# Performance work log

Measured on AMD Instinct MI355X. Metric: run time of the kernel, lower is better.

## Reference

```python
import jax, jax.numpy as jnp
import numpy as np

N, M, C = 262144, 1048576, 32768
ORIG, AF, NF, GH, H, NG = 200, 64, 32, 16, 128, 3


def setup_inputs() -> dict:
    key = jax.random.key(0)
    ks = jax.random.split(key, 16)
    w = lambda k, s: (jax.random.normal(k, s) * 0.02).astype(jnp.float32)
    d = {}
    d["atom_weights"] = jax.random.uniform(ks[0], (N, 1), dtype=jnp.float32)
    d["orig_atom_fea"] = jax.random.normal(ks[1], (N, ORIG), dtype=jnp.float32)
    d["nbr_fea"] = jax.random.normal(ks[2], (M, NF), dtype=jnp.float32)
    d["self_fea_idx"] = jax.random.randint(ks[3], (M,), 0, N)
    d["nbr_fea_idx"] = jax.random.randint(ks[4], (M,), 0, N)
    d["crystal_atom_idx"] = jnp.sort(jax.random.randint(ks[5], (N,), 0, C))
    d["emb_W"] = w(ks[6], (ORIG, AF)); d["emb_b"] = jnp.zeros((AF,), jnp.float32)
    d["filt_W"] = w(ks[7], (NG, 2 * AF + NF, AF)); d["filt_b"] = jnp.zeros((NG, AF), jnp.float32)
    d["core_W"] = w(ks[8], (NG, 2 * AF + NF, AF)); d["core_b"] = jnp.zeros((NG, AF), jnp.float32)
    d["bn_f_g"] = jnp.ones((NG, AF), jnp.float32); d["bn_f_b"] = jnp.zeros((NG, AF), jnp.float32)
    d["bn_c_g"] = jnp.ones((NG, AF), jnp.float32); d["bn_c_b"] = jnp.zeros((NG, AF), jnp.float32)
    d["bn_o_g"] = jnp.ones((NG, AF), jnp.float32); d["bn_o_b"] = jnp.zeros((NG, AF), jnp.float32)
    d["gate_W1"] = w(ks[9], (AF, GH)); d["gate_b1"] = jnp.zeros((GH,), jnp.float32)
    d["gate_bn_g"] = jnp.ones((GH,), jnp.float32); d["gate_bn_b"] = jnp.zeros((GH,), jnp.float32)
    d["gate_W2"] = w(ks[10], (GH, 1)); d["gate_b2"] = jnp.zeros((1,), jnp.float32)
    d["fc_W"] = w(ks[11], (AF, H)); d["fc_b"] = jnp.zeros((H,), jnp.float32)
    d["fc_bn_g"] = jnp.ones((H,), jnp.float32); d["fc_bn_b"] = jnp.zeros((H,), jnp.float32)
    d["out_W"] = w(ks[12], (H, 1)); d["out_b"] = jnp.zeros((1,), jnp.float32)
    return d


def _bn(x, g, b, eps=1e-5):
    # training-mode BatchNorm1d: batch stats over dim 0, biased variance
    return (x - x.mean(0)) / jnp.sqrt(x.var(0) + eps) * g + b


def reference(atom_weights, orig_atom_fea, nbr_fea, self_fea_idx, nbr_fea_idx, crystal_atom_idx,
              emb_W, emb_b, filt_W, filt_b, core_W, core_b,
              bn_f_g, bn_f_b, bn_c_g, bn_c_b, bn_o_g, bn_o_b,
              gate_W1, gate_b1, gate_bn_g, gate_bn_b, gate_W2, gate_b2,
              fc_W, fc_b, fc_bn_g, fc_bn_b, out_W, out_b):
    atom = orig_atom_fea @ emb_W + emb_b  # (N, AF)
    cnt = jnp.clip(jax.ops.segment_sum(jnp.ones((M,), atom.dtype), self_fea_idx, N), 1.0)
    for i in range(NG):  # message-passing layers
        total = jnp.concatenate([atom[self_fea_idx], atom[nbr_fea_idx], nbr_fea], axis=1)  # (M, 2AF+NF)
        f = jax.nn.sigmoid(_bn(total @ filt_W[i] + filt_b[i], bn_f_g[i], bn_f_b[i]))
        c = jax.nn.softplus(_bn(total @ core_W[i] + core_b[i], bn_c_g[i], bn_c_b[i]))
        mean = jax.ops.segment_sum(f * c, self_fea_idx, N) / cnt[:, None]  # scatter_mean
        atom = jax.nn.softplus(atom + _bn(mean, bn_o_g[i], bn_o_b[i]))
    # GlobalAttention pooling over crystals
    gate = jax.nn.relu(_bn(atom @ gate_W1 + gate_b1, gate_bn_g, gate_bn_b)) @ gate_W2 + gate_b2  # (N,1)
    gmax = jax.ops.segment_max(gate, crystal_atom_idx, C)
    gate = atom_weights * jnp.exp(gate - gmax[crystal_atom_idx])
    gate = gate / (jax.ops.segment_sum(gate, crystal_atom_idx, C)[crystal_atom_idx] + 1e-13)
    crys = jax.ops.segment_sum(gate * atom, crystal_atom_idx, C)  # (C, AF)
    crys = jax.nn.softplus(_bn(crys @ fc_W + fc_b, fc_bn_g, fc_bn_b))
    return crys @ out_W + out_b  # (C, 1)
```

## Files before the change

kernel.cpp:

```cpp
#include <hip/hip_runtime.h>
#include <cstdint>
#include <cstddef>

#define NATOM 262144
#define MEDGE 1048576
#define NCRY  32768

typedef __attribute__((ext_vector_type(8))) short short8v;
typedef __attribute__((ext_vector_type(4))) float f32x4;

__device__ __forceinline__ float4 ld4(const float* p){ return *reinterpret_cast<const float4*>(p); }

__device__ __forceinline__ float softplusf_(float x){
  return fmaxf(x, 0.0f) + log1pf(expf(-fabsf(x)));
}
__device__ __forceinline__ float softplus_fast(float x){
  return fmaxf(x, 0.0f) + __logf(1.0f + __expf(-fabsf(x)));
}
__device__ __forceinline__ float sigmoid_fast(float y){
  return __builtin_amdgcn_rcpf(1.0f + __expf(-y));
}

__device__ __forceinline__ unsigned short rne_bf16(float f){
  unsigned u = __float_as_uint(f);
  unsigned r = u + 0x7FFFu + ((u >> 16) & 1u);
  return (unsigned short)(r >> 16);
}
__device__ __forceinline__ float bfu(short s){
  return __uint_as_float(((unsigned)(unsigned short)s) << 16);
}

__device__ __forceinline__ unsigned fkey(float x){
  unsigned b = __float_as_uint(x);
  return (b & 0x80000000u) ? ~b : (b | 0x80000000u);
}
__device__ __forceinline__ float fkeyinv(unsigned k){
  unsigned b = (k & 0x80000000u) ? (k & 0x7fffffffu) : ~k;
  return __uint_as_float(b);
}

__device__ __forceinline__ void gll16(const void* g, void* l){
  __builtin_amdgcn_global_load_lds((const __attribute__((address_space(1))) unsigned*)g,
                                   (__attribute__((address_space(3))) unsigned*)l, 16, 0, 0);
}

#define CSB 32
__global__ __launch_bounds__(256) void colstage(const float* __restrict__ part,
                                                float* __restrict__ part2, int nb){
  int t = threadIdx.x;
  int rpb = nb / CSB;
  const float* p = part + (size_t)blockIdx.x*rpb*256 + t;
  float s = 0.f;
  #pragma unroll 4
  for (int r = 0; r < rpb; ++r) s += p[(size_t)r*256];
  part2[blockIdx.x*256 + t] = s;
}

__global__ __launch_bounds__(256) void cnt_kernel(const int* __restrict__ sidx, float* __restrict__ cnt){
  for (int m = blockIdx.x*256 + threadIdx.x; m < MEDGE; m += gridDim.x*256)
    atomicAdd(&cnt[sidx[m]], 1.0f);
}
__global__ __launch_bounds__(256) void recip_kernel(float* __restrict__ cnt){
  int n = blockIdx.x*256 + threadIdx.x;
  if (n < NATOM) cnt[n] = 1.0f / fmaxf(cnt[n], 1.0f);
}

__global__ __launch_bounds__(256) void nbrprep(const float* __restrict__ nbr, short* __restrict__ nbr_h){
  for (size_t ch = (size_t)blockIdx.x*256 + threadIdx.x; ch < (size_t)MEDGE*32/8; ch += (size_t)gridDim.x*256){
    const float* s = nbr + ch*8;
    float4 a = ld4(s), b = ld4(s+4);
    float fv[8] = {a.x,a.y,a.z,a.w,b.x,b.y,b.z,b.w};
    unsigned w[4];
    #pragma unroll
    for (int i=0;i<4;i++)
      w[i] = (unsigned)rne_bf16(fv[2*i]) | ((unsigned)rne_bf16(fv[2*i+1]) << 16);
    *(uint4*)(nbr_h + ch*8) = make_uint4(w[0],w[1],w[2],w[3]);
  }
}

__global__ __launch_bounds__(256) void wprep_embed(const float* __restrict__ embW,
                                                   short* __restrict__ Weh, short* __restrict__ Wel){
  int idx = blockIdx.x*256 + threadIdx.x;
  if (idx >= 64*224) return;
  int k = idx % 224, c = idx / 224;
  float w = (k < 200) ? embW[(size_t)k*64 + c] : 0.0f;
  unsigned u = __float_as_uint(w);
  unsigned h = u & 0xFFFF0000u;
  Weh[idx] = (short)(h >> 16);
  Wel[idx] = (short)rne_bf16(w - __uint_as_float(h));
}

__global__ __launch_bounds__(256) void embed_mfma(const float* __restrict__ orig,
                                                  const short* __restrict__ Weh,
                                                  const short* __restrict__ Wel,
                                                  const float* __restrict__ bias,
                                                  short* __restrict__ atom_h,
                                                  short* __restrict__ atom_l){
  __shared__ uint4 ab4[3208];
  char* ab = (char*)ab4;
  int t = threadIdx.x, lane = t & 63, wid = t >> 6;
  int r16 = lane & 15, g = lane >> 4;
  int col = wid*16 + r16;

  short8v Bh[7], Bl[7];
  #pragma unroll
  for (int ks = 0; ks < 7; ks++){
    int o = col*224 + ks*32 + g*8;
    Bh[ks] = *(const short8v*)(Weh + o);
    Bl[ks] = *(const short8v*)(Wel + o);
  }
  float bv = bias[col];
  int n0 = blockIdx.x * 64;
  const char* src = (const char*)orig + (size_t)n0*800;
  #pragma unroll
  for (int i = 0; i < 13; i++){
    int j = wid + i*4;
    if (j < 50) gll16(src + j*1024 + lane*16, ab + j*1024);
  }
  __syncthreads();

  #pragma unroll
  for (int grp = 0; grp < 4; grp++){
    f32x4 acc = {bv, bv, bv, bv};
    const char* arow = ab + (grp*16 + r16)*800;
    #pragma unroll
    for (int ks = 0; ks < 7; ks++){
      short8v ah, al;
      if (ks < 6 || g == 0){
        const float* f = (const float*)(arow + ks*128 + g*32);
        float4 f0 = *(const float4*)f, f1 = *(const float4*)(f+4);
        float fv[8] = {f0.x,f0.y,f0.z,f0.w,f1.x,f1.y,f1.z,f1.w};
        unsigned hw[4], lw[4];
        #pragma unroll
        for (int p = 0; p < 4; p++){
          unsigned ua = __float_as_uint(fv[2*p]), ub = __float_as_uint(fv[2*p+1]);
          unsigned ha = ua & 0xFFFF0000u, hb = ub & 0xFFFF0000u;
          hw[p] = (ha >> 16) | hb;
          lw[p] = (unsigned)rne_bf16(fv[2*p]   - __uint_as_float(ha))
                | ((unsigned)rne_bf16(fv[2*p+1] - __uint_as_float(hb)) << 16);
        }
        ah = __builtin_bit_cast(short8v, make_uint4(hw[0],hw[1],hw[2],hw[3]));
        al = __builtin_bit_cast(short8v, make_uint4(lw[0],lw[1],lw[2],lw[3]));
      } else {
        ah = (short8v)0; al = (short8v)0;
      }
      acc = __builtin_amdgcn_mfma_f32_16x16x32_bf16(ah, Bh[ks], acc, 0, 0, 0);
      acc = __builtin_amdgcn_mfma_f32_16x16x32_bf16(al, Bh[ks], acc, 0, 0, 0);
      acc = __builtin_amdgcn_mfma_f32_16x16x32_bf16(ah, Bl[ks], acc, 0, 0, 0);
    }
    int rowb = n0 + grp*16 + g*4;
    #pragma unroll
    for (int r = 0; r < 4; r++){
      float a = acc[r];
      unsigned u = __float_as_uint(a), h = u & 0xFFFF0000u;
      size_t off = (size_t)(rowb + r)*64 + col;
      atom_h[off] = (short)(h >> 16);
      atom_l[off] = (short)rne_bf16(a - __uint_as_float(h));
    }
  }
}

__global__ __launch_bounds__(256) void wprep(const float* __restrict__ filtW, const float* __restrict__ coreW,
                                             short* __restrict__ Wth, short* __restrict__ Wtl){
  int idx = blockIdx.x*256 + threadIdx.x;
  if (idx >= 3*128*160) return;
  int k = idx % 160; int rest = idx / 160; int c = rest & 127; int layer = rest >> 7;
  float w = (c < 64) ? filtW[((size_t)layer*160 + k)*64 + c] : coreW[((size_t)layer*160 + k)*64 + (c-64)];
  unsigned u = __float_as_uint(w);
  unsigned h = u & 0xFFFF0000u;
  Wth[idx] = (short)(h >> 16);
  Wtl[idx] = (short)rne_bf16(w - __uint_as_float(h));
}

#define NT_PER_BLK 8

#define MFMA_B(A,B,ACC) ACC = __builtin_amdgcn_mfma_f32_16x16x32_bf16(A, B, ACC, 0, 0, 0)

template<int PASS>
__global__ __launch_bounds__(256) void edge_mfma(
    const short* __restrict__ atom_h, const short* __restrict__ atom_l,
    const short* __restrict__ nbr_h,
    const int* __restrict__ sidx, const int* __restrict__ nidx,
    const short* __restrict__ Wth, const short* __restrict__ Wtl,
    const float* __restrict__ bfp, const float* __restrict__ bcp,
    const float* __restrict__ scale, const float* __restrict__ shift,
    float* __restrict__ partial,
    float* __restrict__ meanacc)
{
  __shared__ uint4 xb[2][36*32];
  int t = threadIdx.x, lane = t & 63, wid = t >> 6;
  int r16 = lane & 15, g = lane >> 4;
  int colf = wid*16 + r16, colc = colf + 64;
  int el = lane & 31;

  short8v Bhf[5], Blf[5], Bhc[5], Blc[5];
  {
    const short* wfh = Wth + colf*160;
    const short* wch = Wth + colc*160;
    const short* wfl = Wtl + colf*160;
    const short* wcl = Wtl + colc*160;
    #pragma unroll
    for (int ks = 0; ks < 5; ks++){
      int o = ks*32 + g*8;
      Bhf[ks] = *(const short8v*)(wfh + o);
      Bhc[ks] = *(const short8v*)(wch + o);
      Blf[ks] = *(const short8v*)(wfl + o);
      Blc[ks] = *(const short8v*)(wcl + o);
    }
  }
  float bfv = bfp[colf], bcv = bcp[colf];
  float sf = 0.f, hf = 0.f, sc = 0.f, hc = 0.f;
  if (PASS == 1){ sf = scale[colf]; hf = shift[colf]; sc = scale[colc]; hc = shift[colc]; }
  float s0 = 0.f, q0 = 0.f, s1 = 0.f, q1 = 0.f;

  int tile0 = blockIdx.x * NT_PER_BLK;

  #define STAGE(BUF, TILE, SE, NE)                                              \
  {                                                                             \
    uint4* dst = (uint4*)(BUF);                                                 \
    int e0s_ = (TILE)*32;                                                       \
    _Pragma("unroll")                                                           \
    for (int j = wid; j < 18; j += 4){                                          \
      int c = 2*j + (lane >> 5);                                                \
      const short* src;                                                         \
      if      (c < 8)  src = atom_h + (size_t)(SE)*64 + c*8;                    \
      else if (c < 16) src = atom_h + (size_t)(NE)*64 + (c-8)*8;                \
      else if (c < 20) src = nbr_h + (size_t)(e0s_+el)*32 + (c-16)*8;           \
      else if (c < 28) src = atom_l + (size_t)(SE)*64 + (c-20)*8;               \
      else             src = atom_l + (size_t)(NE)*64 + (c-28)*8;               \
      gll16(src, dst + j*64);                                                   \
    }                                                                           \
  }

  int se, ne;
  { int e = tile0*32 + el; se = sidx[e]; ne = nidx[e]; }
  STAGE(xb[0], tile0, se, ne);
  { int e = (tile0+1)*32 + el; se = sidx[e]; ne = nidx[e]; }

  for (int tt = 0; tt < NT_PER_BLK; ++tt){
    asm volatile("s_waitcnt vmcnt(0)" ::: "memory");
    __builtin_amdgcn_s_barrier();
    if (tt+1 < NT_PER_BLK){
      STAGE(xb[(tt+1)&1], tile0+tt+1, se, ne);
      if (tt+2 < NT_PER_BLK){ int e = (tile0+tt+2)*32 + el; se = sidx[e]; ne = nidx[e]; }
    }
    int e0 = (tile0+tt)*32;
    const char* buf = (const char*)xb[tt & 1];
    #pragma unroll
    for (int grp = 0; grp < 2; ++grp){
      f32x4 accf = {bfv,bfv,bfv,bfv}, accc = {bcv,bcv,bcv,bcv};
      const char* base = buf + (grp*16 + r16)*16;
      #pragma unroll
      for (int ks = 0; ks < 5; ++ks){
        short8v ah = *(const short8v*)(base + (ks*4+g)*512);
        MFMA_B(ah, Bhf[ks], accf); MFMA_B(ah, Bhc[ks], accc);
        MFMA_B(ah, Blf[ks], accf); MFMA_B(ah, Blc[ks], accc);
        if (ks < 4){
          short8v al = *(const short8v*)(base + (20+ks*4+g)*512);
          MFMA_B(al, Bhf[ks], accf); MFMA_B(al, Bhc[ks], accc);
        }
      }
      if (PASS == 0){
        #pragma unroll
        for (int r = 0; r < 4; r++){
          float yf = accf[r], yc = accc[r];
          s0 += yf; q0 += yf*yf; s1 += yc; q1 += yc*yc;
        }
      } else {
        int ebase = e0 + grp*16 + g*4;
        #pragma unroll
        for (int r = 0; r < 4; r++){
          float f  = sigmoid_fast(accf[r]*sf + hf);
          float c2 = softplus_fast(accc[r]*sc + hc);
          atomicAdd(&meanacc[(size_t)sidx[ebase + r]*64 + colf], f*c2);
        }
      }
    }
  }
  #undef STAGE

  if (PASS == 0){
    s0 += __shfl_xor(s0,16); s0 += __shfl_xor(s0,32);
    q0 += __shfl_xor(q0,16); q0 += __shfl_xor(q0,32);
    s1 += __shfl_xor(s1,16); s1 += __shfl_xor(s1,32);
    q1 += __shfl_xor(q1,16); q1 += __shfl_xor(q1,32);
    __syncthreads();
    float* scm = (float*)&xb[0][0];
    if (g == 0)
      *(float4*)&scm[(wid*16 + r16)*4] = make_float4(s0, q0, s1, q1);
    __syncthreads();
    {
      int stat = t >> 7, colx = t & 127;
      int isc = (colx >= 64) ? 1 : 0;
      int cc = colx & 63;
      int v = isc*2 + stat;
      partial[(size_t)blockIdx.x*256 + stat*128 + (colx & 127) - stat*0] =
          scm[((cc>>4)*16 + (cc&15))*4 + v];
    }
  }
}

__global__ void bnfin_kernel(int nf, float invcnt, const float* __restrict__ p2,
                             const float* __restrict__ g, const float* __restrict__ b,
                             float* __restrict__ scale, float* __restrict__ shift){
  int j = threadIdx.x;
  if (j >= nf) return;
  float s = 0.f, q = 0.f;
  #pragma unroll 4
  for (int r = 0; r < CSB; ++r){
    s += p2[r*256 + j];
    q += p2[r*256 + 128 + j];
  }
  float m = s*invcnt;
  float v = fmaxf(q*invcnt - m*m, 0.0f);
  float is = rsqrtf(v + 1e-5f);
  float sc = g[j]*is;
  scale[j] = sc;
  shift[j] = b[j] - m*sc;
}

__global__ void bnfin2_kernel(float invcnt, const float* __restrict__ p2,
                              const float* __restrict__ g0, const float* __restrict__ b0,
                              const float* __restrict__ g1, const float* __restrict__ b1,
                              float* __restrict__ scale, float* __restrict__ shift){
  int j = threadIdx.x;
  float s = 0.f, q = 0.f;
  #pragma unroll 4
  for (int r = 0; r < CSB; ++r){
    s += p2[r*256 + j];
    q += p2[r*256 + 128 + j];
  }
  float m = s*invcnt;
  float v = fmaxf(q*invcnt - m*m, 0.0f);
  float is = rsqrtf(v + 1e-5f);
  float gg = (j < 64) ? g0[j] : g1[j-64];
  float bb = (j < 64) ? b0[j] : b1[j-64];
  float sc = gg*is;
  scale[j] = sc;
  shift[j] = bb - m*sc;
}

__global__ __launch_bounds__(256) void meanbn_stats(const float* __restrict__ recip,
                                                    const float* __restrict__ meanacc,
                                                    float* __restrict__ partial){
  int t = threadIdx.x;
  float s = 0.f, q = 0.f;
  for (size_t idx = (size_t)blockIdx.x*256 + t; idx < (size_t)NATOM*64; idx += (size_t)gridDim.x*256){
    int n = (int)(idx >> 6);
    float v = meanacc[idx]*recip[n];
    s += v; q += v*v;
  }
  __shared__ float red[256][2];
  red[t][0]=s; red[t][1]=q;
  __syncthreads();
  if (t < 64){
    for (int i=1;i<4;i++){ s += red[t+64*i][0]; q += red[t+64*i][1]; }
    partial[(size_t)blockIdx.x*256 + t]       = s;
    partial[(size_t)blockIdx.x*256 + 128 + t] = q;
  }
}

__global__ __launch_bounds__(256) void atom_update(short* __restrict__ atom_h,
                                                   short* __restrict__ atom_l,
                                                   const float* __restrict__ meanacc,
                                                   const float* __restrict__ recip,
                                                   const float* __restrict__ scale,
                                                   const float* __restrict__ shift){
  for (size_t idx = (size_t)blockIdx.x*256 + threadIdx.x; idx < (size_t)NATOM*64; idx += (size_t)gridDim.x*256){
    int n = (int)(idx >> 6), j = (int)(idx & 63);
    float prev = bfu(atom_h[idx]) + bfu(atom_l[idx]);
    float a = softplus_fast(prev + meanacc[idx]*recip[n]*scale[j] + shift[j]);
    unsigned u = __float_as_uint(a), h = u & 0xFFFF0000u;
    atom_h[idx] = (short)(h >> 16);
    atom_l[idx] = (short)rne_bf16(a - __uint_as_float(h));
  }
}

__global__ __launch_bounds__(256, 2) void gate_pass1(const short* __restrict__ atom_h,
                                                     const short* __restrict__ atom_l,
                                                     const float* __restrict__ W1, const float* __restrict__ b1,
                                                     float* __restrict__ hbuf,
                                                     float* __restrict__ partial){
  __shared__ float As[256*65];
  __shared__ float Wl[64*16];
  int t = threadIdx.x;
  *(float4*)&Wl[t*4] = ld4(W1 + t*4);
  const short* hsrc = atom_h + (size_t)blockIdx.x*256*64;
  const short* lsrc = atom_l + (size_t)blockIdx.x*256*64;
  #pragma unroll
  for (int j = 0; j < 8; j++){
    int idx = j*256 + t;
    uint4 hv = *(const uint4*)(hsrc + idx*8);
    uint4 lv = *(const uint4*)(lsrc + idx*8);
    int r = idx >> 3, c = (idx & 7)*8;
    float* d = &As[r*65 + c];
    unsigned hw[4] = {hv.x,hv.y,hv.z,hv.w}, lw[4] = {lv.x,lv.y,lv.z,lv.w};
    #pragma unroll
    for (int i = 0; i < 4; i++){
      d[2*i]   = __uint_as_float(hw[i] << 16)          + __uint_as_float(lw[i] << 16);
      d[2*i+1] = __uint_as_float(hw[i] & 0xFFFF0000u)  + __uint_as_float(lw[i] & 0xFFFF0000u);
    }
  }
  __syncthreads();
  float h[16];
  #pragma unroll
  for (int c=0;c<16;c++) h[c] = b1[c];
  const float* ar = &As[t*65];
  #pragma unroll 8
  for (int k=0;k<64;k++){
    float a = ar[k];
    #pragma unroll
    for (int c=0;c<16;c++) h[c] += a*Wl[k*16+c];
  }
  size_t n = (size_t)blockIdx.x*256 + t;
  #pragma unroll
  for (int c=0;c<16;c+=4)
    *(float4*)&hbuf[n*16+c] = make_float4(h[c],h[c+1],h[c+2],h[c+3]);
  __syncthreads();
  #pragma unroll
  for (int c=0;c<16;c++){
    float v = h[c], v2 = h[c]*h[c];
    for (int off=32; off; off>>=1){ v += __shfl_down(v,off); v2 += __shfl_down(v2,off); }
    if ((t&63)==0){ As[(t>>6)*32 + c] = v; As[(t>>6)*32 + 16 + c] = v2; }
  }
  __syncthreads();
  if (t < 32){
    float v = As[t] + As[32+t] + As[64+t] + As[96+t];
    int col = (t < 16) ? t : (128 + t - 16);
    partial[(size_t)blockIdx.x*256 + col] = v;
  }
}

__global__ __launch_bounds__(256) void gate_pass2(const float* __restrict__ hbuf,
                                                  const float* __restrict__ scale, const float* __restrict__ shift,
                                                  const float* __restrict__ W2, const float* __restrict__ b2,
                                                  const int* __restrict__ cry,
                                                  float* __restrict__ gate, unsigned* __restrict__ gmaxk){
  int n = blockIdx.x*256 + threadIdx.x;
  float g = b2[0];
  #pragma unroll
  for (int c=0;c<16;c+=4){
    float4 hv = ld4(hbuf + (size_t)n*16 + c);
    float4 sc = ld4(scale + c), sh = ld4(shift + c), w = ld4(W2 + c);
    g += fmaxf(hv.x*sc.x+sh.x,0.f)*w.x + fmaxf(hv.y*sc.y+sh.y,0.f)*w.y
       + fmaxf(hv.z*sc.z+sh.z,0.f)*w.z + fmaxf(hv.w*sc.w+sh.w,0.f)*w.w;
  }
  gate[n] = g;
  atomicMax(&gmaxk[cry[n]], fkey(g));
}

__global__ __launch_bounds__(256) void gate_exp(float* __restrict__ gate,
                                                const float* __restrict__ aw,
                                                const int* __restrict__ cry,
                                                const unsigned* __restrict__ gmaxk,
                                                float* __restrict__ gsum){
  int n = blockIdx.x*256 + threadIdx.x;
  if (n < NATOM){
    int c = cry[n];
    float w = aw[n]*expf(gate[n] - fkeyinv(gmaxk[c]));
    gate[n] = w;
    atomicAdd(&gsum[c], w);
  }
}

__global__ __launch_bounds__(256) void crys_acc(const float* __restrict__ gate,
                                                const float* __restrict__ gsum,
                                                const int* __restrict__ cry,
                                                const short* __restrict__ atom_h,
                                                const short* __restrict__ atom_l,
                                                float* __restrict__ crys){
  for (size_t idx = (size_t)blockIdx.x*256 + threadIdx.x; idx < (size_t)NATOM*64; idx += (size_t)gridDim.x*256){
    int n = (int)(idx >> 6), j = (int)(idx & 63);
    int c = cry[n];
    float wn = gate[n] / (gsum[c] + 1e-13f);
    float a = bfu(atom_h[idx]) + bfu(atom_l[idx]);
    atomicAdd(&crys[(size_t)c*64 + j], wn*a);
  }
}

__global__ __launch_bounds__(512) void fc_stats(const float* __restrict__ crys,
                                                const float* __restrict__ fcW, const float* __restrict__ fcb,
                                                float* __restrict__ hid,
                                                float* __restrict__ partial){
  __shared__ float Wl[64*128];
  __shared__ float cb[64][16];
  int t = threadIdx.x;
  for (int j = t; j < 64*32; j += 512)
    *(float4*)&Wl[j*4] = ld4(fcW + j*4);
  int cg = t & 31, cr = t >> 5;
  float4 bias = ld4(fcb + cg*4);
  float ssum[4] = {0,0,0,0}, ssq[4] = {0,0,0,0};
  for (int chunk = blockIdx.x; chunk < NCRY/16; chunk += gridDim.x){
    int c0 = chunk*16;
    __syncthreads();
    for (int j = t; j < 256; j += 512){
      int rr = j & 15, c = j >> 4;
      float4 v = ld4(crys + (size_t)(c0+rr)*64 + c*4);
      int k = c*4;
      cb[k][rr]=v.x; cb[k+1][rr]=v.y; cb[k+2][rr]=v.z; cb[k+3][rr]=v.w;
    }
    __syncthreads();
    float4 acc = bias;
    #pragma unroll 4
    for (int k=0;k<64;k++){
      float a = cb[k][cr];
      float4 w = *(float4*)&Wl[k*128 + cg*4];
      acc.x += a*w.x; acc.y += a*w.y; acc.z += a*w.z; acc.w += a*w.w;
    }
    *(float4*)&hid[(size_t)(c0+cr)*128 + cg*4] = acc;
    ssum[0]+=acc.x; ssum[1]+=acc.y; ssum[2]+=acc.z; ssum[3]+=acc.w;
    ssq[0]+=acc.x*acc.x; ssq[1]+=acc.y*acc.y; ssq[2]+=acc.z*acc.z; ssq[3]+=acc.w*acc.w;
  }
  __syncthreads();
  float* red = Wl;
  #pragma unroll
  for (int q=0;q<4;q++){ red[t*8+q] = ssum[q]; red[t*8+4+q] = ssq[q]; }
  __syncthreads();
  if (t < 128){
    int cgj = t >> 2, q = t & 3;
    float s = 0.f, sq = 0.f;
    for (int cri=0; cri<16; cri++){
      int tt = cri*32 + cgj;
      s  += red[tt*8+q];
      sq += red[tt*8+4+q];
    }
    partial[(size_t)blockIdx.x*256 + t]       = s;
    partial[(size_t)blockIdx.x*256 + 128 + t] = sq;
  }
}

__global__ __launch_bounds__(256) void out_kernel(const float* __restrict__ hid,
                                                  const float* __restrict__ scale, const float* __restrict__ shift,
                                                  const float* __restrict__ outW, const float* __restrict__ outb,
                                                  float* __restrict__ out){
  int c = blockIdx.x*4 + (threadIdx.x >> 6);
  int l = threadIdx.x & 63;
  float v = softplusf_(hid[(size_t)c*128 + l]*scale[l] + shift[l])*outW[l]
          + softplusf_(hid[(size_t)c*128 + 64 + l]*scale[64+l] + shift[64+l])*outW[64+l];
  for (int off=32; off; off >>= 1) v += __shfl_down(v, off);
  if (l == 0) out[c] = v + outb[0];
}

extern "C" void kernel_launch(void* const* d_in, const int* in_sizes, int n_in,
                              void* d_out, int out_size, void* d_ws, size_t ws_size,
                              hipStream_t stream){
  const float* aw    = (const float*)d_in[0];
  const float* orig  = (const float*)d_in[1];
  const float* nbr   = (const float*)d_in[2];
  const int*   sidx  = (const int*)d_in[3];
  const int*   nidx  = (const int*)d_in[4];
  const int*   cry   = (const int*)d_in[5];
  const float* embW  = (const float*)d_in[6];
  const float* embB  = (const float*)d_in[7];
  const float* filtW = (const float*)d_in[8];
  const float* filtB = (const float*)d_in[9];
  const float* coreW = (const float*)d_in[10];
  const float* coreB = (const float*)d_in[11];
  const float* bnfg  = (const float*)d_in[12];
  const float* bnfb  = (const float*)d_in[13];
  const float* bncg  = (const float*)d_in[14];
  const float* bncb  = (const float*)d_in[15];
  const float* bnog  = (const float*)d_in[16];
  const float* bnob  = (const float*)d_in[17];
  const float* gW1   = (const float*)d_in[18];
  const float* gb1   = (const float*)d_in[19];
  const float* gbng  = (const float*)d_in[20];
  const float* gbnb  = (const float*)d_in[21];
  const float* gW2   = (const float*)d_in[22];
  const float* gb2   = (const float*)d_in[23];
  const float* fcW   = (const float*)d_in[24];
  const float* fcb   = (const float*)d_in[25];
  const float* fcbng = (const float*)d_in[26];
  const float* fcbnb = (const float*)d_in[27];
  const float* outW  = (const float*)d_in[28];
  const float* outb  = (const float*)d_in[29];
  float* out = (float*)d_out;

  float* ws      = (float*)d_ws;
  float* meanacc = ws;
  float* cnt     = meanacc + (size_t)NATOM*64;
  float* gate    = cnt     + NATOM;
  float* gmaxk   = gate    + NATOM;
  float* gsum    = gmaxk   + NCRY;
  float* crys    = gsum    + NCRY;
  float* hid     = crys    + (size_t)NCRY*64;
  float* part2   = hid     + (size_t)NCRY*128;
  float* scale   = part2   + 32*256;
  float* shift   = scale   + 128;
  short* wth     = (short*)(shift + 128);
  short* wtl     = wth + 3*128*160;
  float* partial = (float*)(wtl + 3*128*160);
  short* atom_h  = (short*)(partial + 4096*256);
  short* atom_l  = atom_h + (size_t)NATOM*64;
  short* nbr_h   = atom_l + (size_t)NATOM*64;
  short* weh     = nbr_h + (size_t)MEDGE*32;
  short* wel     = weh + 64*224;
  (void)in_sizes; (void)n_in; (void)out_size; (void)ws_size;

  hipMemsetAsync(cnt, 0, NATOM*sizeof(float), stream);
  cnt_kernel<<<2048, 256, 0, stream>>>(sidx, cnt);
  recip_kernel<<<NATOM/256, 256, 0, stream>>>(cnt);
  wprep<<<240, 256, 0, stream>>>(filtW, coreW, wth, wtl);
  wprep_embed<<<56, 256, 0, stream>>>(embW, weh, wel);
  nbrprep<<<2048, 256, 0, stream>>>(nbr, nbr_h);
  embed_mfma<<<NATOM/64, 256, 0, stream>>>(orig, weh, wel, embB, atom_h, atom_l);

  for (int i = 0; i < 3; ++i){
    const short* wthL = wth + (size_t)i*128*160;
    const short* wtlL = wtl + (size_t)i*128*160;
    const float* bf = filtB + i*64;
    const float* bc = coreB + i*64;
    edge_mfma<0><<<4096, 256, 0, stream>>>(atom_h, atom_l, nbr_h, sidx, nidx, wthL, wtlL, bf, bc,
                                           nullptr, nullptr, partial, nullptr);
    colstage<<<CSB, 256, 0, stream>>>(partial, part2, 4096);
    bnfin2_kernel<<<1, 128, 0, stream>>>(1.0f/MEDGE, part2,
                                         bnfg+i*64, bnfb+i*64, bncg+i*64, bncb+i*64, scale, shift);
    hipMemsetAsync(meanacc, 0, (size_t)NATOM*64*sizeof(float), stream);
    edge_mfma<1><<<4096, 256, 0, stream>>>(atom_h, atom_l, nbr_h, sidx, nidx, wthL, wtlL, bf, bc,
                                           scale, shift, nullptr, meanacc);
    meanbn_stats<<<2048, 256, 0, stream>>>(cnt, meanacc, partial);
    colstage<<<CSB, 256, 0, stream>>>(partial, part2, 2048);
    bnfin_kernel<<<1, 64, 0, stream>>>(64, 1.0f/NATOM, part2, bnog+i*64, bnob+i*64, scale, shift);
    atom_update<<<2048, 256, 0, stream>>>(atom_h, atom_l, meanacc, cnt, scale, shift);
  }

  float* hbuf = meanacc;
  gate_pass1<<<NATOM/256, 256, 0, stream>>>(atom_h, atom_l, gW1, gb1, hbuf, partial);
  colstage<<<CSB, 256, 0, stream>>>(partial, part2, NATOM/256);
  bnfin_kernel<<<1, 16, 0, stream>>>(16, 1.0f/NATOM, part2, gbng, gbnb, scale, shift);
  hipMemsetAsync(gmaxk, 0, NCRY*sizeof(unsigned), stream);
  gate_pass2<<<NATOM/256, 256, 0, stream>>>(hbuf, scale, shift, gW2, gb2, cry, gate, (unsigned*)gmaxk);
  hipMemsetAsync(gsum, 0, NCRY*sizeof(float), stream);
  gate_exp<<<NATOM/256, 256, 0, stream>>>(gate, aw, cry, (const unsigned*)gmaxk, gsum);
  hipMemsetAsync(crys, 0, (size_t)NCRY*64*sizeof(float), stream);
  crys_acc<<<4096, 256, 0, stream>>>(gate, gsum, cry, atom_h, atom_l, crys);

  fc_stats<<<1024, 512, 0, stream>>>(crys, fcW, fcb, hid, partial);
  colstage<<<CSB, 256, 0, stream>>>(partial, part2, 1024);
  bnfin_kernel<<<1, 128, 0, stream>>>(128, 1.0f/NCRY, part2, fcbng, fcbnb, scale, shift);
  out_kernel<<<NCRY/4, 256, 0, stream>>>(hid, scale, shift, outW, outb, out);
}
```

Before: 1.597 ms.

## Counting-sort edges by destination atom before message-passing layers

Adds a histogram, a three-stage prefix scan and a ranking scatter that reorder edge indices and bf16 neighbor features by self index. The edge kernels then read the sorted arrays, so gathers of self-atom rows become sequential and the scatter-mean atomics land on nearby addresses. This costs an extra pass over all edge features plus several small launches, and the order within each atom's group is nondeterministic, which can change floating-point summation order.

Measured after the change: 2.279 ms. 42.7% more time.

```diff
diff --git a/kernel.cpp b/kernel.cpp
--- a/kernel.cpp
+++ b/kernel.cpp
@@ -56,13 +56,73 @@
   part2[blockIdx.x*256 + t] = s;
 }
 
-__global__ __launch_bounds__(256) void cnt_kernel(const int* __restrict__ sidx, float* __restrict__ cnt){
+__global__ __launch_bounds__(256) void hist_kernel(const int* __restrict__ sidx, int* __restrict__ cnti){
   for (int m = blockIdx.x*256 + threadIdx.x; m < MEDGE; m += gridDim.x*256)
-    atomicAdd(&cnt[sidx[m]], 1.0f);
-}
-__global__ __launch_bounds__(256) void recip_kernel(float* __restrict__ cnt){
+    atomicAdd(&cnti[sidx[m]], 1);
+}
+
+__global__ __launch_bounds__(256) void scan1(const int* __restrict__ cnti,
+                                             int* __restrict__ loc, int* __restrict__ bsum){
+  __shared__ int sm[256];
+  int t = threadIdx.x;
+  int v = cnti[blockIdx.x*256 + t];
+  sm[t] = v;
+  __syncthreads();
+  for (int off = 1; off < 256; off <<= 1){
+    int x = (t >= off) ? sm[t-off] : 0;
+    __syncthreads();
+    sm[t] += x;
+    __syncthreads();
+  }
+  loc[blockIdx.x*256 + t] = sm[t] - v;
+  if (t == 255) bsum[blockIdx.x] = sm[255];
+}
+
+__global__ __launch_bounds__(256) void scan2(int* __restrict__ bsum){
+  __shared__ int sm[256];
+  int t = threadIdx.x;
+  int v0 = bsum[t*4+0], v1 = bsum[t*4+1], v2 = bsum[t*4+2], v3 = bsum[t*4+3];
+  int tot = v0+v1+v2+v3;
+  sm[t] = tot;
+  __syncthreads();
+  for (int off = 1; off < 256; off <<= 1){
+    int x = (t >= off) ? sm[t-off] : 0;
+    __syncthreads();
+    sm[t] += x;
+    __syncthreads();
+  }
+  int te = sm[t] - tot;
+  bsum[t*4+0] = te;
+  bsum[t*4+1] = te + v0;
+  bsum[t*4+2] = te + v0 + v1;
+  bsum[t*4+3] = te + v0 + v1 + v2;
+}
+
+__global__ __launch_bounds__(256) void scan3(const int* __restrict__ loc, const int* __restrict__ bsum,
+                                             int* __restrict__ base){
+  int i = blockIdx.x*256 + threadIdx.x;
+  base[i] = loc[i] + bsum[i >> 8];
+}
+
+__global__ __launch_bounds__(256) void recip_int(const int* __restrict__ cnti, float* __restrict__ recip){
   int n = blockIdx.x*256 + threadIdx.x;
-  if (n < NATOM) cnt[n] = 1.0f / fmaxf(cnt[n], 1.0f);
+  if (n < NATOM) recip[n] = 1.0f / fmaxf((float)cnti[n], 1.0f);
+}
+
+__global__ __launch_bounds__(256) void rank_kernel(const int* __restrict__ sidx, const int* __restrict__ nidx,
+                                                   const int* __restrict__ base, int* __restrict__ ctr,
+                                                   const short* __restrict__ nbr_h,
+                                                   int* __restrict__ sidx_s, int* __restrict__ nidx_s,
+                                                   short* __restrict__ feap){
+  for (int m = blockIdx.x*256 + threadIdx.x; m < MEDGE; m += gridDim.x*256){
+    int s = sidx[m];
+    int p = base[s] + atomicAdd(&ctr[s], 1);
+    sidx_s[p] = s;
+    nidx_s[p] = nidx[m];
+    const uint4* src = (const uint4*)(nbr_h + (size_t)m*32);
+    uint4* dst = (uint4*)(feap + (size_t)p*32);
+    dst[0]=src[0]; dst[1]=src[1]; dst[2]=src[2]; dst[3]=src[3];
+  }
 }
 
 __global__ __launch_bounds__(256) void nbrprep(const float* __restrict__ nbr, short* __restrict__ nbr_h){
@@ -294,8 +354,7 @@
       int isc = (colx >= 64) ? 1 : 0;
       int cc = colx & 63;
       int v = isc*2 + stat;
-      partial[(size_t)blockIdx.x*256 + stat*128 + (colx & 127) - stat*0] =
-          scm[((cc>>4)*16 + (cc&15))*4 + v];
+      partial[(size_t)blockIdx.x*256 + stat*128 + colx] = scm[((cc>>4)*16 + (cc&15))*4 + v];
     }
   }
 }
@@ -595,14 +654,27 @@
   short* nbr_h   = atom_l + (size_t)NATOM*64;
   short* weh     = nbr_h + (size_t)MEDGE*32;
   short* wel     = weh + 64*224;
+  short* feap    = wel + 64*224;
+  int*   cnti    = (int*)(feap + (size_t)MEDGE*32);
+  int*   loc     = cnti + NATOM;
+  int*   base    = loc + NATOM;
+  int*   ctr     = base + NATOM;
+  int*   bsum    = ctr + NATOM;
+  int*   sidx_s  = bsum + 1024;
+  int*   nidx_s  = sidx_s + MEDGE;
   (void)in_sizes; (void)n_in; (void)out_size; (void)ws_size;
 
-  hipMemsetAsync(cnt, 0, NATOM*sizeof(float), stream);
-  cnt_kernel<<<2048, 256, 0, stream>>>(sidx, cnt);
-  recip_kernel<<<NATOM/256, 256, 0, stream>>>(cnt);
+  hipMemsetAsync(cnti, 0, NATOM*sizeof(int), stream);
+  hipMemsetAsync(ctr, 0, NATOM*sizeof(int), stream);
+  hist_kernel<<<2048, 256, 0, stream>>>(sidx, cnti);
+  scan1<<<NATOM/256, 256, 0, stream>>>(cnti, loc, bsum);
+  scan2<<<1, 256, 0, stream>>>(bsum);
+  scan3<<<NATOM/256, 256, 0, stream>>>(loc, bsum, base);
+  recip_int<<<NATOM/256, 256, 0, stream>>>(cnti, cnt);
   wprep<<<240, 256, 0, stream>>>(filtW, coreW, wth, wtl);
   wprep_embed<<<56, 256, 0, stream>>>(embW, weh, wel);
   nbrprep<<<2048, 256, 0, stream>>>(nbr, nbr_h);
+  rank_kernel<<<2048, 256, 0, stream>>>(sidx, nidx, base, ctr, nbr_h, sidx_s, nidx_s, feap);
   embed_mfma<<<NATOM/64, 256, 0, stream>>>(orig, weh, wel, embB, atom_h, atom_l);
 
   for (int i = 0; i < 3; ++i){
@@ -610,13 +682,13 @@
     const short* wtlL = wtl + (size_t)i*128*160;
     const float* bf = filtB + i*64;
     const float* bc = coreB + i*64;
-    edge_mfma<0><<<4096, 256, 0, stream>>>(atom_h, atom_l, nbr_h, sidx, nidx, wthL, wtlL, bf, bc,
+    edge_mfma<0><<<4096, 256, 0, stream>>>(atom_h, atom_l, feap, sidx_s, nidx_s, wthL, wtlL, bf, bc,
                                            nullptr, nullptr, partial, nullptr);
     colstage<<<CSB, 256, 0, stream>>>(partial, part2, 4096);
     bnfin2_kernel<<<1, 128, 0, stream>>>(1.0f/MEDGE, part2,
                                          bnfg+i*64, bnfb+i*64, bncg+i*64, bncb+i*64, scale, shift);
     hipMemsetAsync(meanacc, 0, (size_t)NATOM*64*sizeof(float), stream);
-    edge_mfma<1><<<4096, 256, 0, stream>>>(atom_h, atom_l, nbr_h, sidx, nidx, wthL, wtlL, bf, bc,
+    edge_mfma<1><<<4096, 256, 0, stream>>>(atom_h, atom_l, feap, sidx_s, nidx_s, wthL, wtlL, bf, bc,
                                            scale, shift, nullptr, meanacc);
     meanbn_stats<<<2048, 256, 0, stream>>>(cnt, meanacc, partial);
     colstage<<<CSB, 256, 0, stream>>>(partial, part2, 2048);
```
